# Performance work log

Hardware: AMD Instinct MI355X
Metric: run time of the kernel (lower is better)

Reference implementation:

```python
import jax, jax.numpy as jnp
import numpy as np

H = 768
NH = 12
HD = H // NH
FF = 3072
EPS = 1e-5
CHUNK = 32  # query chunk for L1 distance to bound memory


def layer_norm(x, g, b):
    mu = jnp.mean(x, axis=-1, keepdims=True)
    var = jnp.mean((x - mu) ** 2, axis=-1, keepdims=True)
    return (x - mu) / jnp.sqrt(var + EPS) * g + b


def l1_distance(Q, K):
    # Q, K: [BH, S, D] -> [BH, S, S], computed in query chunks to avoid
    # materializing the full [BH, S, S, D] broadcast intermediate.
    BH, S, D = Q.shape
    nc = S // CHUNK
    Qc = Q.reshape(BH, nc, CHUNK, D).transpose(1, 0, 2, 3)  # [nc, BH, c, D]

    def f(qc):  # qc: [BH, c, D]
        return jnp.sum(jnp.abs(qc[:, :, None, :] - K[:, None, :, :]), axis=-1)

    d = jax.lax.map(f, Qc)  # [nc, BH, c, S]
    return d.transpose(1, 0, 2, 3).reshape(BH, S, S)


def setup_inputs() -> dict:
    key = jax.random.key(0)
    ks = jax.random.split(key, 12)
    sd = 0.02
    B, S = 2, 1024
    return {
        'hidden_states': jax.random.normal(ks[0], (B, S, H), jnp.float32),
        'ln1_g': jnp.ones((H,), jnp.float32),
        'ln1_b': jnp.zeros((H,), jnp.float32),
        'Wq': jax.random.normal(ks[1], (H, H), jnp.float32) * sd,
        'bq': jnp.zeros((H,), jnp.float32),
        'Wk': jax.random.normal(ks[2], (H, H), jnp.float32) * sd,
        'bk': jnp.zeros((H,), jnp.float32),
        'Wv': jax.random.normal(ks[3], (H, H), jnp.float32) * sd,
        'bv': jnp.zeros((H,), jnp.float32),
        'Wo': jax.random.normal(ks[4], (H, H), jnp.float32) * sd,
        'bo': jnp.zeros((H,), jnp.float32),
        'lam': jnp.asarray(1.0, jnp.float32),
        'ln2_g': jnp.ones((H,), jnp.float32),
        'ln2_b': jnp.zeros((H,), jnp.float32),
        'W1': jax.random.normal(ks[5], (H, FF), jnp.float32) * sd,
        'b1': jnp.zeros((FF,), jnp.float32),
        'W2': jax.random.normal(ks[6], (FF, H), jnp.float32) * sd,
        'b2': jnp.zeros((H,), jnp.float32),
    }


def reference(hidden_states, ln1_g, ln1_b, Wq, bq, Wk, bk, Wv, bv, Wo, bo,
              lam, ln2_g, ln2_b, W1, b1, W2, b2):
    B, S, _ = hidden_states.shape
    scale = 1.0 / np.sqrt(HD)

    residual = hidden_states
    x = layer_norm(hidden_states, ln1_g, ln1_b)

    Q = (x @ Wq + bq).reshape(B, S, NH, HD).transpose(0, 2, 1, 3)  # [B,H,S,D]
    K = (x @ Wk + bk).reshape(B, S, NH, HD).transpose(0, 2, 1, 3)
    V = (x @ Wv + bv).reshape(B, S, NH, HD).transpose(0, 2, 1, 3)

    Qf = Q.reshape(B * NH, S, HD)
    Kf = K.reshape(B * NH, S, HD)
    dist = l1_distance(Qf, Kf).reshape(B, NH, S, S)

    scores = -lam * dist * scale
    attn = jax.nn.softmax(scores, axis=-1)  # [B,H,S,S]

    out = jnp.einsum('bhqk,bhkd->bhqd', attn, V)
    out = out.transpose(0, 2, 1, 3).reshape(B, S, H)
    out = out @ Wo + bo
    out = residual + out

    residual = out
    y = layer_norm(out, ln2_g, ln2_b)
    y = jax.nn.gelu(y @ W1 + b1, approximate=False) @ W2 + b2
    out = residual + y
    return out, attn
```

## Files before the change

kernel.cpp:

```cpp
#include <hip/hip_runtime.h>
#include <cstdint>
#include <cstddef>

#define SB    1024
#define BB    2
#define HH    768
#define NHH   12
#define HDD   64
#define FFF   3072
#define RR    (BB*SB)
#define NQKV  2304

#define QSCALE 42.5f

typedef __attribute__((ext_vector_type(8))) short short8;
typedef __attribute__((ext_vector_type(4))) float f4;

__device__ __forceinline__ unsigned short f2bf(float f) {
  union { float f; unsigned u; } x; x.f = f;
  unsigned r = x.u + 0x7FFFu + ((x.u >> 16) & 1u);
  return (unsigned short)(r >> 16);
}

__device__ __forceinline__ unsigned qz8(float x) {
  int v = (int)rintf(x * QSCALE) + 128;
  v = v < 0 ? 0 : (v > 255 ? 255 : v);
  return (unsigned)v;
}

__device__ __forceinline__ void async16(void* lds, const void* g) {
  __builtin_amdgcn_global_load_lds((const __attribute__((address_space(1))) unsigned int*)g,
                                   (__attribute__((address_space(3))) unsigned int*)lds,
                                   16, 0, 0);
}

__global__ __launch_bounds__(256)
void prep_all(const float* __restrict__ Wq, const float* __restrict__ Wk,
              const float* __restrict__ Wv, const float* __restrict__ Wo,
              const float* __restrict__ W1, const float* __restrict__ W2,
              const float* __restrict__ bq, const float* __restrict__ bk,
              const float* __restrict__ bv,
              const float* __restrict__ hidden, const float* __restrict__ ln1_g,
              const float* __restrict__ ln1_b,
              unsigned short* __restrict__ Wqkv_t, unsigned short* __restrict__ W1t,
              unsigned short* __restrict__ W2t, float* __restrict__ bqkv,
              unsigned short* __restrict__ xb) {
  const int t = blockIdx.x;
  const int tid = threadIdx.x;
  __shared__ float tile[64][65];
  __shared__ float rs[4], rq[4];
  if (t >= 1737) {
    const int row = t - 1737;
    const float* x = hidden + (size_t)row * HH;
    float v0 = x[tid], v1 = x[tid + 256], v2 = x[tid + 512];
    float s = v0 + v1 + v2;
    float q = v0 * v0 + v1 * v1 + v2 * v2;
    #pragma unroll
    for (int o = 32; o >= 1; o >>= 1) { s += __shfl_xor(s, o); q += __shfl_xor(q, o); }
    const int w = tid >> 6;
    if ((tid & 63) == 0) { rs[w] = s; rq[w] = q; }
    __syncthreads();
    s = rs[0] + rs[1] + rs[2] + rs[3];
    q = rq[0] + rq[1] + rq[2] + rq[3];
    float mean = s * (1.0f / HH);
    float rstd = rsqrtf(q * (1.0f / HH) - mean * mean + 1e-5f);
    unsigned short* o0 = xb + (size_t)row * HH;
    o0[tid]       = f2bf((v0 - mean) * rstd * ln1_g[tid]       + ln1_b[tid]);
    o0[tid + 256] = f2bf((v1 - mean) * rstd * ln1_g[tid + 256] + ln1_b[tid + 256]);
    o0[tid + 512] = f2bf((v2 - mean) * rstd * ln1_g[tid + 512] + ln1_b[tid + 512]);
    return;
  }
  if (t >= 1728) {
    int i = (t - 1728) * 256 + tid;
    if (i < NQKV)
      bqkv[i] = (i < HH) ? bq[i] : (i < 2 * HH ? bk[i - HH] : bv[i - 2 * HH]);
    return;
  }
  const float* in; unsigned short* out; int ldin, ldout, r0, c0;
  if (t < 576) {
    int m = t / 144, q = t % 144;
    in = m == 0 ? Wq : (m == 1 ? Wk : (m == 2 ? Wv : Wo));
    out = Wqkv_t + (size_t)m * HH * HH;
    ldin = HH; ldout = HH;
    r0 = (q / 12) * 64; c0 = (q % 12) * 64;
  } else if (t < 1152) {
    int q = t - 576;
    in = W1; out = W1t; ldin = FFF; ldout = HH;
    r0 = (q % 12) * 64; c0 = (q / 12) * 64;
  } else {
    int q = t - 1152;
    in = W2; out = W2t; ldin = HH; ldout = FFF;
    r0 = (q % 48) * 64; c0 = (q / 48) * 64;
  }
  for (int i = tid; i < 4096; i += 256) {
    int r = i >> 6, c = i & 63;
    tile[r][c] = in[(size_t)(r0 + r) * ldin + c0 + c];
  }
  __syncthreads();
  for (int i = tid; i < 4096; i += 256) {
    int cc = i >> 6, rr = i & 63;
    out[(size_t)(c0 + cc) * ldout + r0 + rr] = f2bf(tile[rr][cc]);
  }
}

__global__ __launch_bounds__(256)
void gemm_qkv(const unsigned short* __restrict__ A, const unsigned short* __restrict__ Bt,
              const float* __restrict__ bqkv, unsigned* __restrict__ Qq,
              unsigned* __restrict__ Kq, unsigned short* __restrict__ Vt) {
  __shared__ __align__(16) unsigned char smem[34048];
  unsigned short (*lA)[128 * 32] = (unsigned short (*)[128 * 32])smem;
  unsigned short (*lB)[128 * 32] = (unsigned short (*)[128 * 32])(smem + 16384);
  const unsigned short* Ab = A + (size_t)blockIdx.y * 128 * HH;
  const unsigned short* Bb = Bt + (size_t)blockIdx.x * 128 * HH;
  const int tid = threadIdx.x;
  const int wave = tid >> 6, lane = tid & 63;
  const int wr = wave >> 1, wc = wave & 1;
  const int lo = lane & 15, hi = lane >> 4;

  auto stage = [&](int k0, int buf) {
    #pragma unroll
    for (int i = 0; i < 512; i += 256) {
      int idx = i + tid; int r = idx >> 2, kg = idx & 3;
      async16(&lA[buf][idx * 8], &Ab[(size_t)r * HH + k0 + kg * 8]);
    }
    #pragma unroll
    for (int i = 0; i < 512; i += 256) {
      int idx = i + tid; int r = idx >> 2, kg = idx & 3;
      async16(&lB[buf][idx * 8], &Bb[(size_t)r * HH + k0 + kg * 8]);
    }
  };

  stage(0, 0);
  __syncthreads();
  f4 acc[4][4] = {};
  for (int it = 0; it < 24; it++) {
    const int cur = it & 1;
    if (it + 1 < 24) stage((it + 1) * 32, cur ^ 1);
    short8 af[4], bf[4];
    #pragma unroll
    for (int i = 0; i < 4; i++)
      af[i] = *(const short8*)&lA[cur][(wr * 64 + i * 16 + lo) * 32 + hi * 8];
    #pragma unroll
    for (int j = 0; j < 4; j++)
      bf[j] = *(const short8*)&lB[cur][(wc * 64 + j * 16 + lo) * 32 + hi * 8];
    #pragma unroll
    for (int i = 0; i < 4; i++)
      #pragma unroll
      for (int j = 0; j < 4; j++)
        acc[i][j] = __builtin_amdgcn_mfma_f32_16x16x32_bf16(af[i], bf[j], acc[i][j], 0, 0, 0);
    __syncthreads();
  }

  const int reg = blockIdx.x / 6;
  const int cb = blockIdx.x * 128;
  if (reg < 2) {
    unsigned char* t8 = smem;
    #pragma unroll
    for (int i = 0; i < 4; i++)
      #pragma unroll
      for (int j = 0; j < 4; j++) {
        int col = wc * 64 + j * 16 + lo;
        float bv_ = bqkv[cb + col];
        #pragma unroll
        for (int r = 0; r < 4; r++) {
          int row = wr * 64 + i * 16 + hi * 4 + r;
          t8[row * 132 + col] = (unsigned char)qz8(acc[i][j][r] + bv_);
        }
      }
    __syncthreads();
    const unsigned* t32 = (const unsigned*)smem;
    if (reg == 0) {
      #pragma unroll
      for (int i0 = 0; i0 < 4096; i0 += 256) {
        int idx = i0 + tid;
        int cw = idx & 31, rw = idx >> 5;
        int token = blockIdx.y * 128 + rw;
        Qq[(size_t)token * 192 + blockIdx.x * 32 + cw] = t32[rw * 33 + cw];
      }
    } else {
      #pragma unroll
      for (int i0 = 0; i0 < 4096; i0 += 256) {
        int idx = i0 + tid;
        int rw = idx & 127, cw = idx >> 7;
        int token = blockIdx.y * 128 + rw;
        int b = token >> 10, k = token & 1023;
        int dgG = (blockIdx.x - 6) * 32 + cw;
        Kq[(size_t)((b * NHH + (dgG >> 4)) * 16 + (dgG & 15)) * SB + k] = t32[rw * 33 + cw];
      }
    }
  } else {
    unsigned short* t16 = (unsigned short*)smem;
    #pragma unroll
    for (int i = 0; i < 4; i++)
      #pragma unroll
      for (int j = 0; j < 4; j++) {
        int col = wc * 64 + j * 16 + lo;
        float bv_ = bqkv[cb + col];
        #pragma unroll
        for (int r = 0; r < 4; r++) {
          int row = wr * 64 + i * 16 + hi * 4 + r;
          t16[col * 130 + row] = f2bf(acc[i][j][r] + bv_);
        }
      }
    __syncthreads();
    const unsigned* tv = (const unsigned*)smem;
    unsigned* VtU = (unsigned*)Vt;
    #pragma unroll
    for (int i0 = 0; i0 < 8192; i0 += 256) {
      int idx = i0 + tid;
      int rp = idx & 63, cw = idx >> 6;
      int gcol = (blockIdx.x - 12) * 128 + cw;
      int h = gcol >> 6, d = gcol & 63;
      int b = blockIdx.y >> 3;
      VtU[(size_t)((b * NHH + h) * HDD + d) * 512 + (blockIdx.y & 7) * 64 + rp] =
          tv[cw * 65 + rp];
    }
  }
}

template<int BM, int BN, int WR, int WC, int MODE>
__global__ __launch_bounds__(WR*WC*64)
void gemm_bt(const unsigned short* __restrict__ A, int ldA,
             const unsigned short* __restrict__ Bt, int ldB,
             void* __restrict__ Cv, int ldC,
             const float* __restrict__ bias, const float* __restrict__ res,
             int K) {
  constexpr int T = WR * WC * 64;
  __shared__ unsigned short lA[2][BM * 32];
  __shared__ unsigned short lB[2][BN * 32];
  const unsigned short* Ab = A + (size_t)blockIdx.y * BM * ldA;
  const unsigned short* Bb = Bt + (size_t)blockIdx.x * BN * ldB;
  const long cOff = (long)blockIdx.y * BM * ldC + (long)blockIdx.x * BN;
  const int tid = threadIdx.x;
  const int wave = tid >> 6, lane = tid & 63;
  const int wr = wave / WC, wc = wave % WC;
  const int lo = lane & 15, hi = lane >> 4;

  auto stage = [&](int k0, int buf) {
    #pragma unroll
    for (int i = 0; i < BM * 4; i += T) {
      int idx = i + tid; int r = idx >> 2, kg = idx & 3;
      async16(&lA[buf][idx * 8], &Ab[(size_t)r * ldA + k0 + kg * 8]);
    }
    #pragma unroll
    for (int i = 0; i < BN * 4; i += T) {
      int idx = i + tid; int r = idx >> 2, kg = idx & 3;
      async16(&lB[buf][idx * 8], &Bb[(size_t)r * ldB + k0 + kg * 8]);
    }
  };

  const int nIter = K / 32;
  stage(0, 0);
  __syncthreads();
  f4 acc[4][4] = {};
  for (int it = 0; it < nIter; it++) {
    const int cur = it & 1;
    if (it + 1 < nIter) stage((it + 1) * 32, cur ^ 1);
    short8 af[4], bf[4];
    #pragma unroll
    for (int i = 0; i < 4; i++)
      af[i] = *(const short8*)&lA[cur][(wr * 64 + i * 16 + lo) * 32 + hi * 8];
    #pragma unroll
    for (int j = 0; j < 4; j++)
      bf[j] = *(const short8*)&lB[cur][(wc * 64 + j * 16 + lo) * 32 + hi * 8];
    #pragma unroll
    for (int i = 0; i < 4; i++)
      #pragma unroll
      for (int j = 0; j < 4; j++)
        acc[i][j] = __builtin_amdgcn_mfma_f32_16x16x32_bf16(af[i], bf[j], acc[i][j], 0, 0, 0);
    __syncthreads();
  }
  float* Cf = (float*)Cv;
  unsigned short* Cb = (unsigned short*)Cv;
  const int bc0 = blockIdx.x * BN;
  #pragma unroll
  for (int i = 0; i < 4; i++) {
    #pragma unroll
    for (int j = 0; j < 4; j++) {
      int col = wc * 64 + j * 16 + lo;
      #pragma unroll
      for (int r = 0; r < 4; r++) {
        int row = wr * 64 + i * 16 + hi * 4 + r;
        size_t idx = (size_t)cOff + (size_t)row * ldC + col;
        float v = acc[i][j][r];
        if constexpr (MODE == 2) {
          Cf[idx] = v + bias[bc0 + col] + res[idx];
        } else {
          float tt = v + bias[bc0 + col];
          Cb[idx] = f2bf(0.5f * tt * (1.0f + erff(tt * 0.70710678118654752f)));
        }
      }
    }
  }
}

__global__ __launch_bounds__(256)
void ln_kernel(const float* __restrict__ in, const float* __restrict__ g,
               const float* __restrict__ bb, unsigned short* __restrict__ out) {
  const int row = blockIdx.x, tid = threadIdx.x;
  const float* x = in + (size_t)row * HH;
  float v0 = x[tid], v1 = x[tid + 256], v2 = x[tid + 512];
  float s = v0 + v1 + v2;
  float q = v0 * v0 + v1 * v1 + v2 * v2;
  #pragma unroll
  for (int o = 32; o >= 1; o >>= 1) { s += __shfl_xor(s, o); q += __shfl_xor(q, o); }
  __shared__ float rs[4], rq[4];
  const int w = tid >> 6;
  if ((tid & 63) == 0) { rs[w] = s; rq[w] = q; }
  __syncthreads();
  s = rs[0] + rs[1] + rs[2] + rs[3];
  q = rq[0] + rq[1] + rq[2] + rq[3];
  float mean = s * (1.0f / HH);
  float rstd = rsqrtf(q * (1.0f / HH) - mean * mean + 1e-5f);
  unsigned short* o0 = out + (size_t)row * HH;
  o0[tid]       = f2bf((v0 - mean) * rstd * g[tid]       + bb[tid]);
  o0[tid + 256] = f2bf((v1 - mean) * rstd * g[tid + 256] + bb[tid + 256]);
  o0[tid + 512] = f2bf((v2 - mean) * rstd * g[tid + 512] + bb[tid + 512]);
}

#define DQ 16
__global__ __launch_bounds__(512)
void dist_softmax_pv(const unsigned* __restrict__ Qq, const unsigned* __restrict__ Kq,
                     const unsigned short* __restrict__ Vt,
                     const float* __restrict__ lam_p,
                     float* __restrict__ attnF, unsigned short* __restrict__ ctx) {
  __shared__ __align__(16) unsigned lk[8 * SB];
  __shared__ unsigned lq[DQ * 16];
  const int bh = blockIdx.y;
  const int q0 = blockIdx.x * DQ;
  const int b = bh / NHH, h = bh % NHH;
  const int tid = threadIdx.x;
  const int w = tid >> 6, lane = tid & 63;
  const int lo = lane & 15, hi = lane >> 4;

  if (tid < 256) {
    int r = tid >> 4, dg = tid & 15;
    lq[r * 16 + dg] = Qq[(size_t)(b * SB + q0 + r) * 192 + h * 16 + dg];
  }

  const unsigned* Ks = Kq + (size_t)bh * 16 * SB;
  unsigned acc[2][4][4] = {};
  const unsigned* lqw = &lq[(w * 2) * 16];

  #pragma unroll
  for (int ch = 0; ch < 2; ch++) {
    #pragma unroll
    for (int i = 0; i < 4; i++)
      async16(&lk[(i * 512 + tid) * 4], Ks + (size_t)ch * 8192 + (i * 512 + tid) * 4);
    __syncthreads();
    #pragma unroll
    for (int dg = 0; dg < 8; dg++) {
      unsigned qd[2];
      #pragma unroll
      for (int qi = 0; qi < 2; qi++) qd[qi] = lqw[qi * 16 + ch * 8 + dg];
      uint4 kv[4];
      #pragma unroll
      for (int kg = 0; kg < 4; kg++)
        kv[kg] = *(const uint4*)&lk[dg * SB + kg * 256 + lane * 4];
      #pragma unroll
      for (int qi = 0; qi < 2; qi++) {
        #pragma unroll
        for (int kg = 0; kg < 4; kg++) {
          acc[qi][kg][0] = __builtin_amdgcn_sad_u8(qd[qi], kv[kg].x, acc[qi][kg][0]);
          acc[qi][kg][1] = __builtin_amdgcn_sad_u8(qd[qi], kv[kg].y, acc[qi][kg][1]);
          acc[qi][kg][2] = __builtin_amdgcn_sad_u8(qd[qi], kv[kg].z, acc[qi][kg][2]);
          acc[qi][kg][3] = __builtin_amdgcn_sad_u8(qd[qi], kv[kg].w, acc[qi][kg][3]);
        }
      }
    }
    __syncthreads();
  }

  unsigned short* lp = (unsigned short*)lk;
  const float kscl = -lam_p[0] * 0.125f / QSCALE;
  #pragma unroll
  for (int qi = 0; qi < 2; qi++) {
    float sc[16];
    float m = -1e30f;
    #pragma unroll
    for (int kg = 0; kg < 4; kg++)
      #pragma unroll
      for (int c = 0; c < 4; c++) {
        float v = (float)acc[qi][kg][c] * kscl;
        sc[kg * 4 + c] = v;
        m = fmaxf(m, v);
      }
    #pragma unroll
    for (int off = 1; off < 64; off <<= 1) m = fmaxf(m, __shfl_xor(m, off));
    float s = 0.f;
    #pragma unroll
    for (int i = 0; i < 16; i++) {
      float e = __expf(sc[i] - m);
      sc[i] = e;
      s += e;
    }
    #pragma unroll
    for (int off = 1; off < 64; off <<= 1) s += __shfl_xor(s, off);
    const float rinv = 1.0f / s;
    const int row = w * 2 + qi;
    const size_t gb = (size_t)bh * SB * SB + (size_t)(q0 + row) * SB + lane * 4;
    #pragma unroll
    for (int kg = 0; kg < 4; kg++) {
      float4 p;
      p.x = sc[kg * 4 + 0] * rinv;
      p.y = sc[kg * 4 + 1] * rinv;
      p.z = sc[kg * 4 + 2] * rinv;
      p.w = sc[kg * 4 + 3] * rinv;
      *(float4*)&attnF[gb + kg * 256] = p;
      ushort4 pb;
      pb.x = f2bf(p.x); pb.y = f2bf(p.y); pb.z = f2bf(p.z); pb.w = f2bf(p.w);
      *(ushort4*)&lp[row * SB + kg * 256 + lane * 4] = pb;
    }
  }
  __syncthreads();

  if (w < 4) {
    const unsigned short* Vb = Vt + ((size_t)bh * HDD + w * 16 + lo) * SB + hi * 8;
    const unsigned short* Pb = lp + lo * SB + hi * 8;
    f4 cacc = {0.f, 0.f, 0.f, 0.f};
    #pragma unroll
    for (int k0 = 0; k0 < SB; k0 += 32) {
      short8 af = *(const short8*)(Pb + k0);
      short8 bf = *(const short8*)(Vb + k0);
      cacc = __builtin_amdgcn_mfma_f32_16x16x32_bf16(af, bf, cacc, 0, 0, 0);
    }
    unsigned short* cb = ctx + (size_t)(b * SB + q0 + hi * 4) * HH + h * HDD + w * 16 + lo;
    #pragma unroll
    for (int r = 0; r < 4; r++) cb[(size_t)r * HH] = f2bf(cacc[r]);
  }
}

extern "C" void kernel_launch(void* const* d_in, const int* in_sizes, int n_in,
                              void* d_out, int out_size, void* d_ws, size_t ws_size,
                              hipStream_t stream) {
  (void)in_sizes; (void)n_in; (void)out_size; (void)ws_size;
  const float* hidden = (const float*)d_in[0];
  const float* ln1_g  = (const float*)d_in[1];
  const float* ln1_b  = (const float*)d_in[2];
  const float* Wq     = (const float*)d_in[3];
  const float* bq     = (const float*)d_in[4];
  const float* Wk     = (const float*)d_in[5];
  const float* bk     = (const float*)d_in[6];
  const float* Wv     = (const float*)d_in[7];
  const float* bv     = (const float*)d_in[8];
  const float* Wo     = (const float*)d_in[9];
  const float* bo     = (const float*)d_in[10];
  const float* lam    = (const float*)d_in[11];
  const float* ln2_g  = (const float*)d_in[12];
  const float* ln2_b  = (const float*)d_in[13];
  const float* W1     = (const float*)d_in[14];
  const float* b1     = (const float*)d_in[15];
  const float* W2     = (const float*)d_in[16];
  const float* b2     = (const float*)d_in[17];

  float* out0  = (float*)d_out;
  float* attnF = out0 + (size_t)RR * HH;

  char* w = (char*)d_ws;
  auto alloc = [&](size_t bytes) { char* p = w; w += (bytes + 255) & ~(size_t)255; return p; };
  unsigned short* xb      = (unsigned short*)alloc((size_t)RR * HH * 2);
  unsigned short* Wqkv_t  = (unsigned short*)alloc((size_t)NQKV * HH * 2);
  unsigned short* Wo_t    = (unsigned short*)alloc((size_t)HH * HH * 2);
  unsigned short* W1t     = (unsigned short*)alloc((size_t)FFF * HH * 2);
  unsigned short* W2t     = (unsigned short*)alloc((size_t)HH * FFF * 2);
  float*          bqkv    = (float*)alloc((size_t)NQKV * 4);
  unsigned*       Qq      = (unsigned*)alloc((size_t)RR * 192 * 4);
  unsigned*       Kq      = (unsigned*)alloc((size_t)BB * NHH * 16 * SB * 4);
  unsigned short* Vt      = (unsigned short*)alloc((size_t)BB * NHH * HDD * SB * 2);
  unsigned short* ctx     = (unsigned short*)alloc((size_t)RR * HH * 2);
  float*          attnOut = (float*)alloc((size_t)RR * HH * 4);
  unsigned short* h1      = (unsigned short*)alloc((size_t)RR * FFF * 2);
  unsigned short* y2      = Vt;

  prep_all<<<dim3(1737 + RR), 256, 0, stream>>>(Wq, Wk, Wv, Wo, W1, W2, bq, bk, bv,
                                                hidden, ln1_g, ln1_b,
                                                Wqkv_t, W1t, W2t, bqkv, xb);

  gemm_qkv<<<dim3(NQKV / 128, RR / 128), 256, 0, stream>>>(
      xb, Wqkv_t, bqkv, Qq, Kq, Vt);

  dist_softmax_pv<<<dim3(SB / DQ, BB * NHH), 512, 0, stream>>>(
      Qq, Kq, Vt, lam, attnF, ctx);

  gemm_bt<64, 64, 1, 1, 2><<<dim3(HH / 64, RR / 64), 64, 0, stream>>>(
      ctx, HH, Wo_t, HH, attnOut, HH, bo, hidden, HH);

  ln_kernel<<<dim3(RR), 256, 0, stream>>>(attnOut, ln2_g, ln2_b, y2);

  gemm_bt<128, 128, 2, 2, 3><<<dim3(FFF / 128, RR / 128), 256, 0, stream>>>(
      y2, HH, W1t, HH, h1, FFF, b1, nullptr, HH);

  gemm_bt<64, 64, 1, 1, 2><<<dim3(HH / 64, RR / 64), 64, 0, stream>>>(
      h1, FFF, W2t, FFF, out0, HH, b2, attnOut, FFF);
}
```

Measured before the change: 317.5 us.

## Use split-K 128x128 GEMMs for Wo and W2 with fused reduce/bias/residual/LN

The output-projection and FFN-down GEMMs now use 128x128 tiles with four waves and a four-way split-K over grid z. Each split writes fp32 partials to a workspace buffer. New reduction kernels sum the partials and add bias and residual, and for Wo they also apply LayerNorm 2. The goal is to replace the old single-wave 64x64 tiles, which gave little MFMA reuse and too few waves per CU, with larger tiles while still keeping enough blocks in flight. The cost is extra global traffic for the four fp32 partial buffers, plus a separate reduction pass.

```diff
diff --git a/kernel.cpp b/kernel.cpp
--- a/kernel.cpp
+++ b/kernel.cpp
@@ -218,19 +218,22 @@
   }
 }
 
-template<int BM, int BN, int WR, int WC, int MODE>
+template<int BM, int BN, int WR, int WC, int MODE, int KS>
 __global__ __launch_bounds__(WR*WC*64)
 void gemm_bt(const unsigned short* __restrict__ A, int ldA,
              const unsigned short* __restrict__ Bt, int ldB,
              void* __restrict__ Cv, int ldC,
-             const float* __restrict__ bias, const float* __restrict__ res,
-             int K) {
+             const float* __restrict__ bias,
+             int K, long partStride) {
   constexpr int T = WR * WC * 64;
   __shared__ unsigned short lA[2][BM * 32];
   __shared__ unsigned short lB[2][BN * 32];
-  const unsigned short* Ab = A + (size_t)blockIdx.y * BM * ldA;
-  const unsigned short* Bb = Bt + (size_t)blockIdx.x * BN * ldB;
-  const long cOff = (long)blockIdx.y * BM * ldC + (long)blockIdx.x * BN;
+  const int ks = blockIdx.z;
+  const int KH = K / KS;
+  const unsigned short* Ab = A + (size_t)blockIdx.y * BM * ldA + (size_t)ks * KH;
+  const unsigned short* Bb = Bt + (size_t)blockIdx.x * BN * ldB + (size_t)ks * KH;
+  const long cOff = (long)blockIdx.y * BM * ldC + (long)blockIdx.x * BN
+                  + (long)ks * partStride;
   const int tid = threadIdx.x;
   const int wave = tid >> 6, lane = tid & 63;
   const int wr = wave / WC, wc = wave % WC;
@@ -249,7 +252,7 @@
     }
   };
 
-  const int nIter = K / 32;
+  const int nIter = KH / 32;
   stage(0, 0);
   __syncthreads();
   f4 acc[4][4] = {};
@@ -283,11 +286,11 @@
         int row = wr * 64 + i * 16 + hi * 4 + r;
         size_t idx = (size_t)cOff + (size_t)row * ldC + col;
         float v = acc[i][j][r];
-        if constexpr (MODE == 2) {
-          Cf[idx] = v + bias[bc0 + col] + res[idx];
-        } else {
+        if constexpr (MODE == 3) {
           float tt = v + bias[bc0 + col];
           Cb[idx] = f2bf(0.5f * tt * (1.0f + erff(tt * 0.70710678118654752f)));
+        } else {
+          Cf[idx] = v;
         }
       }
     }
@@ -295,13 +298,22 @@
 }
 
 __global__ __launch_bounds__(256)
-void ln_kernel(const float* __restrict__ in, const float* __restrict__ g,
-               const float* __restrict__ bb, unsigned short* __restrict__ out) {
+void reduce_ln(const float* __restrict__ p, const float* __restrict__ bias,
+               const float* __restrict__ res, const float* __restrict__ g,
+               const float* __restrict__ bb, float* __restrict__ attnOut,
+               unsigned short* __restrict__ out) {
   const int row = blockIdx.x, tid = threadIdx.x;
-  const float* x = in + (size_t)row * HH;
-  float v0 = x[tid], v1 = x[tid + 256], v2 = x[tid + 512];
-  float s = v0 + v1 + v2;
-  float q = v0 * v0 + v1 * v1 + v2 * v2;
+  const size_t rb = (size_t)row * HH;
+  float v[3]; float s = 0.f, q = 0.f;
+  #pragma unroll
+  for (int j = 0; j < 3; j++) {
+    int c = tid + j * 256;
+    size_t idx = rb + c;
+    float a = p[idx] + p[(size_t)RR * HH + idx] + p[2 * (size_t)RR * HH + idx]
+            + p[3 * (size_t)RR * HH + idx] + bias[c] + res[idx];
+    attnOut[idx] = a;
+    v[j] = a; s += a; q += a * a;
+  }
   #pragma unroll
   for (int o = 32; o >= 1; o >>= 1) { s += __shfl_xor(s, o); q += __shfl_xor(q, o); }
   __shared__ float rs[4], rq[4];
@@ -312,10 +324,32 @@
   q = rq[0] + rq[1] + rq[2] + rq[3];
   float mean = s * (1.0f / HH);
   float rstd = rsqrtf(q * (1.0f / HH) - mean * mean + 1e-5f);
-  unsigned short* o0 = out + (size_t)row * HH;
-  o0[tid]       = f2bf((v0 - mean) * rstd * g[tid]       + bb[tid]);
-  o0[tid + 256] = f2bf((v1 - mean) * rstd * g[tid + 256] + bb[tid + 256]);
-  o0[tid + 512] = f2bf((v2 - mean) * rstd * g[tid + 512] + bb[tid + 512]);
+  #pragma unroll
+  for (int j = 0; j < 3; j++) {
+    int c = tid + j * 256;
+    out[rb + c] = f2bf((v[j] - mean) * rstd * g[c] + bb[c]);
+  }
+}
+
+__global__ __launch_bounds__(256)
+void reduce4_bias_res(const float* __restrict__ p, const float* __restrict__ bias,
+                      const float* __restrict__ res, float* __restrict__ out) {
+  int i = (blockIdx.x * 256 + threadIdx.x) * 4;
+  int col = i % HH;
+  float4 a = *(const float4*)(p + i);
+  #pragma unroll
+  for (int s = 1; s < 4; s++) {
+    float4 b = *(const float4*)(p + (size_t)s * RR * HH + i);
+    a.x += b.x; a.y += b.y; a.z += b.z; a.w += b.w;
+  }
+  float4 bb = *(const float4*)(bias + col);
+  float4 r = *(const float4*)(res + i);
+  float4 o;
+  o.x = a.x + bb.x + r.x;
+  o.y = a.y + bb.y + r.y;
+  o.z = a.z + bb.z + r.z;
+  o.w = a.w + bb.w + r.w;
+  *(float4*)(out + i) = o;
 }
 
 #define DQ 16
@@ -470,7 +504,9 @@
   unsigned short* ctx     = (unsigned short*)alloc((size_t)RR * HH * 2);
   float*          attnOut = (float*)alloc((size_t)RR * HH * 4);
   unsigned short* h1      = (unsigned short*)alloc((size_t)RR * FFF * 2);
+  float*          gPart   = (float*)alloc((size_t)4 * RR * HH * 4);
   unsigned short* y2      = Vt;
+  (void)Wo_t;
 
   prep_all<<<dim3(1737 + RR), 256, 0, stream>>>(Wq, Wk, Wv, Wo, W1, W2, bq, bk, bv,
                                                 hidden, ln1_g, ln1_b,
@@ -482,14 +518,18 @@
   dist_softmax_pv<<<dim3(SB / DQ, BB * NHH), 512, 0, stream>>>(
       Qq, Kq, Vt, lam, attnF, ctx);
 
-  gemm_bt<64, 64, 1, 1, 2><<<dim3(HH / 64, RR / 64), 64, 0, stream>>>(
-      ctx, HH, Wo_t, HH, attnOut, HH, bo, hidden, HH);
-
-  ln_kernel<<<dim3(RR), 256, 0, stream>>>(attnOut, ln2_g, ln2_b, y2);
-
-  gemm_bt<128, 128, 2, 2, 3><<<dim3(FFF / 128, RR / 128), 256, 0, stream>>>(
-      y2, HH, W1t, HH, h1, FFF, b1, nullptr, HH);
-
-  gemm_bt<64, 64, 1, 1, 2><<<dim3(HH / 64, RR / 64), 64, 0, stream>>>(
-      h1, FFF, W2t, FFF, out0, HH, b2, attnOut, FFF);
-}
+  gemm_bt<128, 128, 2, 2, 4, 4><<<dim3(HH / 128, RR / 128, 4), 256, 0, stream>>>(
+      ctx, HH, Wqkv_t + (size_t)3 * HH * HH, HH, gPart, HH,
+      nullptr, HH, (long)RR * HH);
+
+  reduce_ln<<<dim3(RR), 256, 0, stream>>>(gPart, bo, hidden, ln2_g, ln2_b,
+                                          attnOut, y2);
+
+  gemm_bt<128, 128, 2, 2, 3, 1><<<dim3(FFF / 128, RR / 128, 1), 256, 0, stream>>>(
+      y2, HH, W1t, HH, h1, FFF, b1, HH, 0);
+
+  gemm_bt<128, 128, 2, 2, 4, 4><<<dim3(HH / 128, RR / 128, 4), 256, 0, stream>>>(
+      h1, FFF, W2t, FFF, gPart, HH, nullptr, FFF, (long)RR * HH);
+
+  reduce4_bias_res<<<dim3(RR * HH / 1024), 256, 0, stream>>>(gPart, b2, attnOut, out0);
+}
```

New measurement: 291.9 us. 1.09x faster.
